# Kernel tuning notes

Hardware: AMD Instinct MI355X
Metric: run time of the kernel (lower is better)

The kernel has to match this reference:

```python
import jax, jax.numpy as jnp
import numpy as np
from jax import lax

STRIDE, PAD, K = 1, 1, 3  # module defaults


def setup_inputs() -> dict:
    key = jax.random.key(0)
    k1, k2, k3, k4 = jax.random.split(key, 4)
    N, C, H, W, O = 8, 64, 112, 112, 64
    n = K * K
    x = jax.random.normal(k1, (N, C, H, W), jnp.float32)
    # kaiming-uniform-ish scale for main conv weight
    weight = jax.random.normal(k2, (O, C, K, K), jnp.float32) * (1.0 / np.sqrt(C * K * K))
    bias = jnp.zeros((O,), jnp.float32)
    # small random offset predictor (original zero-inits; small values exercise bilinear path)
    offset_w = jax.random.normal(k3, (3 * n, C, K, K), jnp.float32) * 0.01
    offset_b = jax.random.normal(k4, (3 * n,), jnp.float32) * 0.01
    return {"x": x, "weight": weight, "bias": bias, "offset_w": offset_w, "offset_b": offset_b}


def _bilinear(x, py, px):
    """Zero-padded bilinear sampling. x:[N,C,H,W]; py,px:[N,n,Ho,Wo] -> [N,C,n,Ho,Wo]."""
    N, C, H, W = x.shape
    xf = x.reshape(N, C, H * W)
    y0 = jnp.floor(py)
    x0 = jnp.floor(px)
    out = jnp.zeros((N, C) + py.shape[1:], x.dtype)
    for dy in (0.0, 1.0):
        for dx in (0.0, 1.0):
            yi = y0 + dy
            xi = x0 + dx
            w = (1.0 - jnp.abs(py - yi)) * (1.0 - jnp.abs(px - xi))
            valid = (yi >= 0) & (yi <= H - 1) & (xi >= 0) & (xi <= W - 1)
            yc = jnp.clip(yi, 0, H - 1).astype(jnp.int32)
            xc = jnp.clip(xi, 0, W - 1).astype(jnp.int32)
            idx = (yc * W + xc).reshape(N, 1, -1)
            g = jnp.take_along_axis(xf, jnp.broadcast_to(idx, (N, C, idx.shape[-1])), axis=2)
            g = g.reshape((N, C) + py.shape[1:])
            out = out + g * jnp.where(valid, w, 0.0)[:, None]
    return out


def reference(x, weight, bias, offset_w, offset_b):
    N, C, H, W = x.shape
    O = weight.shape[0]
    n = K * K
    # offset/mask predictor: 3x3 conv -> [N, 3*n, Ho, Wo]
    raw = lax.conv_general_dilated(
        x, offset_w, (STRIDE, STRIDE), [(PAD, PAD), (PAD, PAD)],
        dimension_numbers=("NCHW", "OIHW", "NCHW"),
    ) + offset_b[None, :, None, None]
    Ho, Wo = raw.shape[2], raw.shape[3]
    off = raw[:, : 2 * n].reshape(N, n, 2, Ho, Wo)       # (dy, dx) per tap
    mask = jax.nn.sigmoid(raw[:, 2 * n :])               # [N, n, Ho, Wo]
    # base sampling grid: p0 + kernel tap position
    tap_y = (jnp.arange(n) // K).astype(jnp.float32)[:, None, None]   # [n,1,1]
    tap_x = (jnp.arange(n) % K).astype(jnp.float32)[:, None, None]
    base_y = (jnp.arange(Ho) * STRIDE - PAD).astype(jnp.float32)[None, :, None] + tap_y  # [n,Ho,1]
    base_x = (jnp.arange(Wo) * STRIDE - PAD).astype(jnp.float32)[None, None, :] + tap_x  # [n,1,Wo]
    py = off[:, :, 0] + base_y[None]   # [N,n,Ho,Wo]
    px = off[:, :, 1] + base_x[None]
    sampled = _bilinear(x, py, px)                       # [N,C,n,Ho,Wo]
    val = sampled * mask[:, None]                        # modulation
    out = jnp.einsum("ncthw,oct->nohw", val, weight.reshape(O, C, n))
    return out + bias[None, :, None, None]
```

## Files before the change

### kernel.cpp

```cpp
#include <hip/hip_runtime.h>
#include <hip/hip_fp16.h>
#include <math.h>

#define NB  8
#define CIN 64
#define HH  112
#define WW  112
#define OC  64
#define HWSZ (HH*WW)
#define NPOS (NB*HWSZ)

#define PR 9
#define PC 22
#define NPOSP (PR*PC)
#define PATCH_CHUNKS (NPOSP*8)

typedef unsigned short u16;
typedef __attribute__((ext_vector_type(8))) _Float16 h8;
typedef __attribute__((ext_vector_type(4))) float floatx4;

#define XT_ELEMS   (NB*HWSZ*CIN)
#define WSWZ_ELEMS (18*4*64*8)
#define OSWZ_ELEMS (18*4*32*8)

union CV { uint4 u; h8 h; };

__device__ __forceinline__ u16 f2h(float f) { return __half_as_ushort(__float2half(f)); }
__device__ __forceinline__ __half2 H2(unsigned v) { union { unsigned u; __half2 h; } c; c.u = v; return c.h; }
__device__ __forceinline__ unsigned U2(__half2 h) { union { unsigned u; __half2 h; } c; c.h = h; return c.u; }
__device__ __forceinline__ unsigned pkh(float lo, float hi) {
    union { __half2 h; unsigned u; } c;
    c.h = __floats2half2_rn(lo, hi);
    return c.u;
}

struct TapW { __half2 w00, w01, w10, w11; };

__global__ __launch_bounds__(256) void transpose_k(
    const float* __restrict__ x, u16* __restrict__ xt)
{
    __shared__ float t[64][65];
    const int n   = blockIdx.y;
    const int hw0 = blockIdx.x * 64;
    const int tid = threadIdx.x;
    const int wv  = tid & 63;
    const int g   = tid >> 6;
    #pragma unroll
    for (int i = 0; i < 16; ++i) {
        const int c = i*4 + g;
        t[c][wv] = x[((size_t)n*CIN + c)*HWSZ + hw0 + wv];
    }
    __syncthreads();
    #pragma unroll
    for (int i = 0; i < 4; ++i) {
        const int unit = i*256 + tid;
        const int cg = unit & 15;
        const int hw = unit >> 4;
        uint2 o;
        o.x = pkh(t[cg*4+0][hw], t[cg*4+1][hw]);
        o.y = pkh(t[cg*4+2][hw], t[cg*4+3][hw]);
        *(uint2*)(xt + ((size_t)n*HWSZ + hw0 + hw)*CIN + cg*4) = o;
    }
}

__global__ __launch_bounds__(256) void wswz_k(
    const float* __restrict__ wgt, const float* __restrict__ offw,
    u16* __restrict__ wswz, u16* __restrict__ oswz)
{
    const int gid = blockIdx.x * 256 + threadIdx.x;
    if (gid < WSWZ_ELEMS) {
        const int j = gid & 7, o = (gid >> 3) & 63, q = (gid >> 9) & 3, s = gid >> 11;
        const int k = s*32 + q*8 + j;
        const int c = k & 63, t = k >> 6;
        wswz[gid] = f2h(wgt[o*576 + c*9 + t]);
    } else {
        const int g2 = gid - WSWZ_ELEMS;
        const int j = g2 & 7, r = (g2 >> 3) & 31, q = (g2 >> 8) & 3, s = g2 >> 10;
        const int k = s*32 + q*8 + j;
        const int c = k & 63, t = k >> 6;
        oswz[g2] = (r < 27) ? f2h(offw[r*576 + c*9 + t]) : (u16)0;
    }
}

#define IML(DST, S_) { \
    const int t_ = (S_) >> 1; \
    const int ty_ = t_/3, tx_ = t_ - 3*ty_; \
    const int r_ = wid + 1 + ty_; \
    const int c_ = m + 1 + tx_; \
    const int pos_ = r_*PC + c_; \
    const int ck_ = ((S_) & 1)*4 + q; \
    DST = *(const uint4*)(patch + pos_*128 + ((ck_ ^ (pos_ & 7)) << 4)); }

#define OFF_MFMA(SRC, S_) { CV cb_; cb_.u = (SRC); \
    const u16* ap_ = oswz + ((S_)*4 + q)*256 + m*8; \
    acc0 = __builtin_amdgcn_mfma_f32_16x16x32_f16(*(const h8*)(ap_),       cb_.h, acc0, 0, 0, 0); \
    acc1 = __builtin_amdgcn_mfma_f32_16x16x32_f16(*(const h8*)(ap_ + 128), cb_.h, acc1, 0, 0, 0); }

#define HALF_STEP(R00, R01, R10, R11, TW, S_) { \
    CV cb_; \
    cb_.u.x = U2(__hfma2(H2((R00).x),(TW).w00, __hfma2(H2((R01).x),(TW).w01, \
              __hfma2(H2((R10).x),(TW).w10, __hmul2(H2((R11).x),(TW).w11))))); \
    cb_.u.y = U2(__hfma2(H2((R00).y),(TW).w00, __hfma2(H2((R01).y),(TW).w01, \
              __hfma2(H2((R10).y),(TW).w10, __hmul2(H2((R11).y),(TW).w11))))); \
    cb_.u.z = U2(__hfma2(H2((R00).z),(TW).w00, __hfma2(H2((R01).z),(TW).w01, \
              __hfma2(H2((R10).z),(TW).w10, __hmul2(H2((R11).z),(TW).w11))))); \
    cb_.u.w = U2(__hfma2(H2((R00).w),(TW).w00, __hfma2(H2((R01).w),(TW).w01, \
              __hfma2(H2((R10).w),(TW).w10, __hmul2(H2((R11).w),(TW).w11))))); \
    const u16* wp_ = wswz + ((S_)*4 + q)*512 + m*8; \
    acc[0] = __builtin_amdgcn_mfma_f32_16x16x32_f16(*(const h8*)(wp_),       cb_.h, acc[0], 0, 0, 0); \
    acc[1] = __builtin_amdgcn_mfma_f32_16x16x32_f16(*(const h8*)(wp_ + 128), cb_.h, acc[1], 0, 0, 0); \
    acc[2] = __builtin_amdgcn_mfma_f32_16x16x32_f16(*(const h8*)(wp_ + 256), cb_.h, acc[2], 0, 0, 0); \
    acc[3] = __builtin_amdgcn_mfma_f32_16x16x32_f16(*(const h8*)(wp_ + 384), cb_.h, acc[3], 0, 0, 0); }

__global__ __launch_bounds__(256)
void dcn_k(
    const u16*  __restrict__ xt,
    const u16*  __restrict__ wswz,
    const u16*  __restrict__ oswz,
    const float* __restrict__ bias,
    const float* __restrict__ offb,
    float* __restrict__ out)
{
    __shared__ uint4 patch4[PATCH_CHUNKS];
    __shared__ float raws[4][32][16];
    __shared__ uint2 prmW[4][9][16];
    __shared__ unsigned prmO[4][9][16];
    char* patch = (char*)patch4;

    const int tid  = threadIdx.x;
    const int lane = tid & 63;
    const int wid  = tid >> 6;
    const int m    = lane & 15;
    const int q    = lane >> 4;

    const int n   = blockIdx.x & 7;
    const int idx = blockIdx.x >> 3;
    const int rg  = idx / 7;
    const int cc  = idx - rg*7;
    const int hoB = rg * 4;
    const int wo0 = cc * 16;
    const int ho  = hoB + wid;
    const u16* xtn = xt + (size_t)n * HWSZ * CIN;

    #pragma unroll
    for (int i = 0; i < 7; ++i) {
        const int u = i*256 + tid;
        if (u < PATCH_CHUNKS) {
            const int pos = u >> 3, ck = u & 7;
            const int pry = pos / PC;
            const int pcx = pos - pry*PC;
            const int gy = hoB - 2 + pry;
            const int gx = wo0 - 2 + pcx;
            uint4 v = {0u,0u,0u,0u};
            if (((unsigned)gy < HH) && ((unsigned)gx < WW))
                v = *(const uint4*)(xtn + (gy*WW + gx)*CIN + ck*8);
            *(uint4*)(patch + pos*128 + ((ck ^ (pos & 7)) << 4)) = v;
        }
    }
    __syncthreads();

    {
        uint4 b[6];
        floatx4 acc0 = {0.f,0.f,0.f,0.f}, acc1 = {0.f,0.f,0.f,0.f};
        #pragma unroll
        for (int s = 0; s < 6; ++s) IML(b[s], s)
        #pragma unroll
        for (int s = 0; s < 6; ++s) {
            uint4 nv; IML(nv, s + 6)
            OFF_MFMA(b[s], s)
            b[s] = nv;
        }
        #pragma unroll
        for (int s = 0; s < 6; ++s) {
            uint4 nv; IML(nv, s + 12)
            OFF_MFMA(b[s], s + 6)
            b[s] = nv;
        }
        #pragma unroll
        for (int s = 0; s < 6; ++s) OFF_MFMA(b[s], s + 12)

        #pragma unroll
        for (int r = 0; r < 4; ++r) {
            raws[wid][q*4 + r][m]      = acc0[r];
            raws[wid][16 + q*4 + r][m] = acc1[r];
        }
    }
    __syncthreads();

    #pragma unroll
    for (int i = 0; i < 3; ++i) {
        const int e = i*64 + lane;
        if (e < 144) {
            const int t = e >> 4;
            const int p = e & 15;
            const int ty = t / 3, tx = t - 3*ty;
            const float py = raws[wid][2*t][p]     + offb[2*t]     + (float)(ho - 1 + ty);
            const float px = raws[wid][2*t + 1][p] + offb[2*t + 1] + (float)(wo0 + p - 1 + tx);
            const float mk = 1.f / (1.f + expf(-(raws[wid][18 + t][p] + offb[18 + t])));
            const float y0f = floorf(py), x0f = floorf(px);
            const float fy = py - y0f, fx = px - x0f;
            const int y0 = (int)y0f, x0 = (int)x0f;
            const float gy = 1.f - fy, gx = 1.f - fx;
            const bool vy0 = (unsigned)y0       < HH;
            const bool vy1 = (unsigned)(y0 + 1) < HH;
            const bool vx0 = (unsigned)x0       < WW;
            const bool vx1 = (unsigned)(x0 + 1) < WW;
            const float w00 = (vy0 && vx0) ? gy*gx*mk : 0.f;
            const float w01 = (vy0 && vx1) ? gy*fx*mk : 0.f;
            const float w10 = (vy1 && vx0) ? fy*gx*mk : 0.f;
            const float w11 = (vy1 && vx1) ? fy*fx*mk : 0.f;
            const int yc0 = min(max(y0, 0), HH-1),  yc1 = min(max(y0+1, 0), HH-1);
            const int xc0 = min(max(x0, 0), WW-1),  xc1 = min(max(x0+1, 0), WW-1);
            const unsigned o00 = (unsigned)((yc0*WW + xc0)*CIN);
            const unsigned dxb = (unsigned)(xc1 - xc0);
            const unsigned dyb = (unsigned)(yc1 - yc0);
            const int r0  = yc0 - (hoB - 2);
            const int c0l = xc0 - (wo0 - 2);
            const bool inp = (r0 >= 0) && (r0 + (int)dyb <= PR-1)
                          && (c0l >= 0) && (c0l + (int)dxb <= PC-1);
            const int pos00 = r0*PC + c0l;
            prmO[wid][t][p] = o00 | (dxb << 20) | (dyb << 21)
                            | (((unsigned)pos00 & 0xFFu) << 22)
                            | (inp ? (1u << 30) : 0u);
            uint2 Wv;
            Wv.x = (unsigned)__half_as_ushort(__float2half(w00))
                 | ((unsigned)__half_as_ushort(__float2half(w01)) << 16);
            Wv.y = (unsigned)__half_as_ushort(__float2half(w10))
                 | ((unsigned)__half_as_ushort(__float2half(w11)) << 16);
            prmW[wid][t][p] = Wv;
        }
    }
    __syncthreads();

    floatx4 acc[4];
    #pragma unroll
    for (int i = 0; i < 4; ++i) acc[i] = (floatx4){0.f,0.f,0.f,0.f};

    const int ch0 = q*8, ch1 = 32 + q*8;

    #pragma unroll
    for (int t = 0; t < 9; ++t) {
        const unsigned Po = prmO[wid][t][m];
        const uint2  Pw = prmW[wid][t][m];
        TapW tw;
        tw.w00 = __half2half2(__ushort_as_half((u16)(Pw.x & 0xFFFFu)));
        tw.w01 = __half2half2(__ushort_as_half((u16)(Pw.x >> 16)));
        tw.w10 = __half2half2(__ushort_as_half((u16)(Pw.y & 0xFFFFu)));
        tw.w11 = __half2half2(__ushort_as_half((u16)(Pw.y >> 16)));
        uint4 g0,g1,g2,g3,g4,g5,g6,g7;
        if (__all((int)((Po >> 30) & 1u))) {
            const int p00 = (int)((Po >> 22) & 0xFFu);
            const int dxb = (int)((Po >> 20) & 1u);
            const int dyb = (int)((Po >> 21) & 1u);
            const int p01 = p00 + dxb;
            const int p10 = p00 + dyb*PC;
            const int p11 = p10 + dxb;
            const int a00 = p00*128 + ((q ^ (p00 & 7)) << 4);
            const int a01 = p01*128 + ((q ^ (p01 & 7)) << 4);
            const int a10 = p10*128 + ((q ^ (p10 & 7)) << 4);
            const int a11 = p11*128 + ((q ^ (p11 & 7)) << 4);
            g0 = *(const uint4*)(patch + a00);
            g1 = *(const uint4*)(patch + a01);
            g2 = *(const uint4*)(patch + a10);
            g3 = *(const uint4*)(patch + a11);
            g4 = *(const uint4*)(patch + (a00 ^ 64));
            g5 = *(const uint4*)(patch + (a01 ^ 64));
            g6 = *(const uint4*)(patch + (a10 ^ 64));
            g7 = *(const uint4*)(patch + (a11 ^ 64));
        } else {
            const int o00 = (int)(Po & 0xFFFFFu);
            const int dx  = (int)((Po >> 20) & 1u) << 6;
            const int dy  = (int)((Po >> 21) & 1u) * (WW*CIN);
            g0 = *(const uint4*)(xtn + o00 + ch0);
            g1 = *(const uint4*)(xtn + o00 + dx + ch0);
            g2 = *(const uint4*)(xtn + o00 + dy + ch0);
            g3 = *(const uint4*)(xtn + o00 + dx + dy + ch0);
            g4 = *(const uint4*)(xtn + o00 + ch1);
            g5 = *(const uint4*)(xtn + o00 + dx + ch1);
            g6 = *(const uint4*)(xtn + o00 + dy + ch1);
            g7 = *(const uint4*)(xtn + o00 + dx + dy + ch1);
        }
        HALF_STEP(g0, g1, g2, g3, tw, 2*t)
        HALF_STEP(g4, g5, g6, g7, tw, 2*t + 1)
    }

    #pragma unroll
    for (int ob = 0; ob < 4; ++ob) {
        #pragma unroll
        for (int r = 0; r < 4; ++r) {
            const int o = ob*16 + q*4 + r;
            out[(((size_t)n*OC + o)*HH + ho)*WW + wo0 + m] = acc[ob][r] + bias[o];
        }
    }
}

extern "C" void kernel_launch(void* const* d_in, const int* in_sizes, int n_in,
                              void* d_out, int out_size, void* d_ws, size_t ws_size,
                              hipStream_t stream)
{
    const float* x    = (const float*)d_in[0];
    const float* wgt  = (const float*)d_in[1];
    const float* bias = (const float*)d_in[2];
    const float* offw = (const float*)d_in[3];
    const float* offb = (const float*)d_in[4];
    float* out = (float*)d_out;

    u16* xt   = (u16*)d_ws;
    u16* wswz = xt + XT_ELEMS;
    u16* oswz = wswz + WSWZ_ELEMS;

    transpose_k<<<dim3(HWSZ/64, NB), 256, 0, stream>>>(x, xt);
    wswz_k<<<dim3((WSWZ_ELEMS + OSWZ_ELEMS)/256), 256, 0, stream>>>(wgt, offw, wswz, oswz);
    dcn_k<<<dim3(NPOS/64), 256, 0, stream>>>(xt, wswz, oswz, bias, offb, out);
}
```

Baseline: 130.6 us.

## Merge prep kernels, shrink patch halo, alias LDS buffers, add fast in-patch path

Measured after the change: 114.8 us. 12.1% less time.

```diff
diff --git a/kernel.cpp b/kernel.cpp
--- a/kernel.cpp
+++ b/kernel.cpp
@@ -10,10 +10,12 @@
 #define HWSZ (HH*WW)
 #define NPOS (NB*HWSZ)
 
-#define PR 9
-#define PC 22
+#define PR 8
+#define PC 21
 #define NPOSP (PR*PC)
 #define PATCH_CHUNKS (NPOSP*8)
+
+#define TP_BLOCKS (HWSZ/64*NB)
 
 typedef unsigned short u16;
 typedef __attribute__((ext_vector_type(8))) _Float16 h8;
@@ -36,49 +38,49 @@
 
 struct TapW { __half2 w00, w01, w10, w11; };
 
-__global__ __launch_bounds__(256) void transpose_k(
-    const float* __restrict__ x, u16* __restrict__ xt)
+__global__ __launch_bounds__(256) void prep_k(
+    const float* __restrict__ x, const float* __restrict__ wgt,
+    const float* __restrict__ offw,
+    u16* __restrict__ xt, u16* __restrict__ wswz, u16* __restrict__ oswz)
 {
     __shared__ float t[64][65];
-    const int n   = blockIdx.y;
-    const int hw0 = blockIdx.x * 64;
     const int tid = threadIdx.x;
-    const int wv  = tid & 63;
-    const int g   = tid >> 6;
-    #pragma unroll
-    for (int i = 0; i < 16; ++i) {
-        const int c = i*4 + g;
-        t[c][wv] = x[((size_t)n*CIN + c)*HWSZ + hw0 + wv];
-    }
-    __syncthreads();
-    #pragma unroll
-    for (int i = 0; i < 4; ++i) {
-        const int unit = i*256 + tid;
-        const int cg = unit & 15;
-        const int hw = unit >> 4;
-        uint2 o;
-        o.x = pkh(t[cg*4+0][hw], t[cg*4+1][hw]);
-        o.y = pkh(t[cg*4+2][hw], t[cg*4+3][hw]);
-        *(uint2*)(xt + ((size_t)n*HWSZ + hw0 + hw)*CIN + cg*4) = o;
-    }
-}
-
-__global__ __launch_bounds__(256) void wswz_k(
-    const float* __restrict__ wgt, const float* __restrict__ offw,
-    u16* __restrict__ wswz, u16* __restrict__ oswz)
-{
-    const int gid = blockIdx.x * 256 + threadIdx.x;
-    if (gid < WSWZ_ELEMS) {
-        const int j = gid & 7, o = (gid >> 3) & 63, q = (gid >> 9) & 3, s = gid >> 11;
-        const int k = s*32 + q*8 + j;
-        const int c = k & 63, t = k >> 6;
-        wswz[gid] = f2h(wgt[o*576 + c*9 + t]);
+    const int bid = blockIdx.x;
+    if (bid < TP_BLOCKS) {
+        const int n   = bid & 7;
+        const int hw0 = (bid >> 3) * 64;
+        const int wv  = tid & 63;
+        const int g   = tid >> 6;
+        #pragma unroll
+        for (int i = 0; i < 16; ++i) {
+            const int c = i*4 + g;
+            t[c][wv] = x[((size_t)n*CIN + c)*HWSZ + hw0 + wv];
+        }
+        __syncthreads();
+        #pragma unroll
+        for (int i = 0; i < 4; ++i) {
+            const int unit = i*256 + tid;
+            const int cg = unit & 15;
+            const int hw = unit >> 4;
+            uint2 o;
+            o.x = pkh(t[cg*4+0][hw], t[cg*4+1][hw]);
+            o.y = pkh(t[cg*4+2][hw], t[cg*4+3][hw]);
+            *(uint2*)(xt + ((size_t)n*HWSZ + hw0 + hw)*CIN + cg*4) = o;
+        }
     } else {
-        const int g2 = gid - WSWZ_ELEMS;
-        const int j = g2 & 7, r = (g2 >> 3) & 31, q = (g2 >> 8) & 3, s = g2 >> 10;
-        const int k = s*32 + q*8 + j;
-        const int c = k & 63, t = k >> 6;
-        oswz[g2] = (r < 27) ? f2h(offw[r*576 + c*9 + t]) : (u16)0;
+        const int gid = (bid - TP_BLOCKS)*256 + tid;
+        if (gid < WSWZ_ELEMS) {
+            const int j = gid & 7, o = (gid >> 3) & 63, q = (gid >> 9) & 3, s = gid >> 11;
+            const int k = s*32 + q*8 + j;
+            const int c = k & 63, tt = k >> 6;
+            wswz[gid] = f2h(wgt[o*576 + c*9 + tt]);
+        } else {
+            const int g2 = gid - WSWZ_ELEMS;
+            const int j = g2 & 7, r = (g2 >> 3) & 31, q = (g2 >> 8) & 3, s = g2 >> 10;
+            const int k = s*32 + q*8 + j;
+            const int c = k & 63, tt = k >> 6;
+            oswz[g2] = (r < 27) ? f2h(offw[r*576 + c*9 + tt]) : (u16)0;
+        }
     }
 }
 
@@ -112,7 +114,14 @@
     acc[2] = __builtin_amdgcn_mfma_f32_16x16x32_f16(*(const h8*)(wp_ + 256), cb_.h, acc[2], 0, 0, 0); \
     acc[3] = __builtin_amdgcn_mfma_f32_16x16x32_f16(*(const h8*)(wp_ + 384), cb_.h, acc[3], 0, 0, 0); }
 
+#define UNPACK_TW(TW, PW) { \
+    (TW).w00 = __half2half2(__ushort_as_half((u16)((PW).x & 0xFFFFu))); \
+    (TW).w01 = __half2half2(__ushort_as_half((u16)((PW).x >> 16))); \
+    (TW).w10 = __half2half2(__ushort_as_half((u16)((PW).y & 0xFFFFu))); \
+    (TW).w11 = __half2half2(__ushort_as_half((u16)((PW).y >> 16))); }
+
 __global__ __launch_bounds__(256)
+__attribute__((amdgpu_waves_per_eu(5, 8)))
 void dcn_k(
     const u16*  __restrict__ xt,
     const u16*  __restrict__ wswz,
@@ -122,10 +131,10 @@
     float* __restrict__ out)
 {
     __shared__ uint4 patch4[PATCH_CHUNKS];
-    __shared__ float raws[4][32][16];
-    __shared__ uint2 prmW[4][9][16];
-    __shared__ unsigned prmO[4][9][16];
+    __shared__ float rawsm[4][32][16];
     char* patch = (char*)patch4;
+    uint2*    prmW = (uint2*)rawsm;
+    unsigned* prmO = (unsigned*)((char*)rawsm + 4608);
 
     const int tid  = threadIdx.x;
     const int lane = tid & 63;
@@ -143,7 +152,7 @@
     const u16* xtn = xt + (size_t)n * HWSZ * CIN;
 
     #pragma unroll
-    for (int i = 0; i < 7; ++i) {
+    for (int i = 0; i < 6; ++i) {
         const int u = i*256 + tid;
         if (u < PATCH_CHUNKS) {
             const int pos = u >> 3, ck = u & 7;
@@ -181,12 +190,24 @@
 
         #pragma unroll
         for (int r = 0; r < 4; ++r) {
-            raws[wid][q*4 + r][m]      = acc0[r];
-            raws[wid][16 + q*4 + r][m] = acc1[r];
+            rawsm[wid][q*4 + r][m]      = acc0[r];
+            rawsm[wid][16 + q*4 + r][m] = acc1[r];
         }
     }
     __syncthreads();
 
+    float vy[3], vx[3], vmk[3];
+    #pragma unroll
+    for (int i = 0; i < 3; ++i) {
+        const int e = i*64 + lane;
+        if (e < 144) {
+            const int t = e >> 4, p = e & 15;
+            vy[i]  = rawsm[wid][2*t][p];
+            vx[i]  = rawsm[wid][2*t + 1][p];
+            vmk[i] = rawsm[wid][18 + t][p];
+        }
+    }
+    __syncthreads();
     #pragma unroll
     for (int i = 0; i < 3; ++i) {
         const int e = i*64 + lane;
@@ -194,9 +215,9 @@
             const int t = e >> 4;
             const int p = e & 15;
             const int ty = t / 3, tx = t - 3*ty;
-            const float py = raws[wid][2*t][p]     + offb[2*t]     + (float)(ho - 1 + ty);
-            const float px = raws[wid][2*t + 1][p] + offb[2*t + 1] + (float)(wo0 + p - 1 + tx);
-            const float mk = 1.f / (1.f + expf(-(raws[wid][18 + t][p] + offb[18 + t])));
+            const float py = vy[i] + offb[2*t]     + (float)(ho - 1 + ty);
+            const float px = vx[i] + offb[2*t + 1] + (float)(wo0 + p - 1 + tx);
+            const float mk = 1.f / (1.f + expf(-(vmk[i] + offb[18 + t])));
             const float y0f = floorf(py), x0f = floorf(px);
             const float fy = py - y0f, fx = px - x0f;
             const int y0 = (int)y0f, x0 = (int)x0f;
@@ -219,7 +240,7 @@
             const bool inp = (r0 >= 0) && (r0 + (int)dyb <= PR-1)
                           && (c0l >= 0) && (c0l + (int)dxb <= PC-1);
             const int pos00 = r0*PC + c0l;
-            prmO[wid][t][p] = o00 | (dxb << 20) | (dyb << 21)
+            prmO[(wid*9 + t)*16 + p] = o00 | (dxb << 20) | (dyb << 21)
                             | (((unsigned)pos00 & 0xFFu) << 22)
                             | (inp ? (1u << 30) : 0u);
             uint2 Wv;
@@ -227,7 +248,7 @@
                  | ((unsigned)__half_as_ushort(__float2half(w01)) << 16);
             Wv.y = (unsigned)__half_as_ushort(__float2half(w10))
                  | ((unsigned)__half_as_ushort(__float2half(w11)) << 16);
-            prmW[wid][t][p] = Wv;
+            prmW[(wid*9 + t)*16 + p] = Wv;
         }
     }
     __syncthreads();
@@ -236,19 +257,20 @@
     #pragma unroll
     for (int i = 0; i < 4; ++i) acc[i] = (floatx4){0.f,0.f,0.f,0.f};
 
-    const int ch0 = q*8, ch1 = 32 + q*8;
-
-    #pragma unroll
-    for (int t = 0; t < 9; ++t) {
-        const unsigned Po = prmO[wid][t][m];
-        const uint2  Pw = prmW[wid][t][m];
-        TapW tw;
-        tw.w00 = __half2half2(__ushort_as_half((u16)(Pw.x & 0xFFFFu)));
-        tw.w01 = __half2half2(__ushort_as_half((u16)(Pw.x >> 16)));
-        tw.w10 = __half2half2(__ushort_as_half((u16)(Pw.y & 0xFFFFu)));
-        tw.w11 = __half2half2(__ushort_as_half((u16)(Pw.y >> 16)));
-        uint4 g0,g1,g2,g3,g4,g5,g6,g7;
-        if (__all((int)((Po >> 30) & 1u))) {
+    const unsigned* PoB = prmO + wid*9*16 + m;
+    const uint2*    PwB = prmW + wid*9*16 + m;
+
+    unsigned band = 0xFFFFFFFFu;
+    #pragma unroll
+    for (int t = 0; t < 9; ++t) band &= PoB[t*16];
+
+    if (__all((int)((band >> 30) & 1u))) {
+        unsigned Po = PoB[0];
+        uint2    Pw = PwB[0];
+        #pragma unroll
+        for (int t = 0; t < 9; ++t) {
+            const unsigned PoN = (t < 8) ? PoB[(t+1)*16] : 0u;
+            const uint2    PwN = (t < 8) ? PwB[(t+1)*16] : Pw;
             const int p00 = (int)((Po >> 22) & 0xFFu);
             const int dxb = (int)((Po >> 20) & 1u);
             const int dyb = (int)((Po >> 21) & 1u);
@@ -259,29 +281,62 @@
             const int a01 = p01*128 + ((q ^ (p01 & 7)) << 4);
             const int a10 = p10*128 + ((q ^ (p10 & 7)) << 4);
             const int a11 = p11*128 + ((q ^ (p11 & 7)) << 4);
-            g0 = *(const uint4*)(patch + a00);
-            g1 = *(const uint4*)(patch + a01);
-            g2 = *(const uint4*)(patch + a10);
-            g3 = *(const uint4*)(patch + a11);
-            g4 = *(const uint4*)(patch + (a00 ^ 64));
-            g5 = *(const uint4*)(patch + (a01 ^ 64));
-            g6 = *(const uint4*)(patch + (a10 ^ 64));
-            g7 = *(const uint4*)(patch + (a11 ^ 64));
-        } else {
-            const int o00 = (int)(Po & 0xFFFFFu);
-            const int dx  = (int)((Po >> 20) & 1u) << 6;
-            const int dy  = (int)((Po >> 21) & 1u) * (WW*CIN);
-            g0 = *(const uint4*)(xtn + o00 + ch0);
-            g1 = *(const uint4*)(xtn + o00 + dx + ch0);
-            g2 = *(const uint4*)(xtn + o00 + dy + ch0);
-            g3 = *(const uint4*)(xtn + o00 + dx + dy + ch0);
-            g4 = *(const uint4*)(xtn + o00 + ch1);
-            g5 = *(const uint4*)(xtn + o00 + dx + ch1);
-            g6 = *(const uint4*)(xtn + o00 + dy + ch1);
-            g7 = *(const uint4*)(xtn + o00 + dx + dy + ch1);
-        }
-        HALF_STEP(g0, g1, g2, g3, tw, 2*t)
-        HALF_STEP(g4, g5, g6, g7, tw, 2*t + 1)
+            const uint4 g0 = *(const uint4*)(patch + a00);
+            const uint4 g1 = *(const uint4*)(patch + a01);
+            const uint4 g2 = *(const uint4*)(patch + a10);
+            const uint4 g3 = *(const uint4*)(patch + a11);
+            const uint4 g4 = *(const uint4*)(patch + (a00 ^ 64));
+            const uint4 g5 = *(const uint4*)(patch + (a01 ^ 64));
+            const uint4 g6 = *(const uint4*)(patch + (a10 ^ 64));
+            const uint4 g7 = *(const uint4*)(patch + (a11 ^ 64));
+            TapW tw; UNPACK_TW(tw, Pw)
+            HALF_STEP(g0, g1, g2, g3, tw, 2*t)
+            HALF_STEP(g4, g5, g6, g7, tw, 2*t + 1)
+            Po = PoN; Pw = PwN;
+        }
+    } else {
+        const int ch0 = q*8, ch1 = 32 + q*8;
+        #pragma unroll
+        for (int t = 0; t < 9; ++t) {
+            const unsigned Po = PoB[t*16];
+            const uint2    Pw = PwB[t*16];
+            TapW tw; UNPACK_TW(tw, Pw)
+            uint4 g0,g1,g2,g3,g4,g5,g6,g7;
+            if (__all((int)((Po >> 30) & 1u))) {
+                const int p00 = (int)((Po >> 22) & 0xFFu);
+                const int dxb = (int)((Po >> 20) & 1u);
+                const int dyb = (int)((Po >> 21) & 1u);
+                const int p01 = p00 + dxb;
+                const int p10 = p00 + dyb*PC;
+                const int p11 = p10 + dxb;
+                const int a00 = p00*128 + ((q ^ (p00 & 7)) << 4);
+                const int a01 = p01*128 + ((q ^ (p01 & 7)) << 4);
+                const int a10 = p10*128 + ((q ^ (p10 & 7)) << 4);
+                const int a11 = p11*128 + ((q ^ (p11 & 7)) << 4);
+                g0 = *(const uint4*)(patch + a00);
+                g1 = *(const uint4*)(patch + a01);
+                g2 = *(const uint4*)(patch + a10);
+                g3 = *(const uint4*)(patch + a11);
+                g4 = *(const uint4*)(patch + (a00 ^ 64));
+                g5 = *(const uint4*)(patch + (a01 ^ 64));
+                g6 = *(const uint4*)(patch + (a10 ^ 64));
+                g7 = *(const uint4*)(patch + (a11 ^ 64));
+            } else {
+                const int o00 = (int)(Po & 0xFFFFFu);
+                const int dx  = (int)((Po >> 20) & 1u) << 6;
+                const int dy  = (int)((Po >> 21) & 1u) * (WW*CIN);
+                g0 = *(const uint4*)(xtn + o00 + ch0);
+                g1 = *(const uint4*)(xtn + o00 + dx + ch0);
+                g2 = *(const uint4*)(xtn + o00 + dy + ch0);
+                g3 = *(const uint4*)(xtn + o00 + dx + dy + ch0);
+                g4 = *(const uint4*)(xtn + o00 + ch1);
+                g5 = *(const uint4*)(xtn + o00 + dx + ch1);
+                g6 = *(const uint4*)(xtn + o00 + dy + ch1);
+                g7 = *(const uint4*)(xtn + o00 + dx + dy + ch1);
+            }
+            HALF_STEP(g0, g1, g2, g3, tw, 2*t)
+            HALF_STEP(g4, g5, g6, g7, tw, 2*t + 1)
+        }
     }
 
     #pragma unroll
@@ -309,7 +364,7 @@
     u16* wswz = xt + XT_ELEMS;
     u16* oswz = wswz + WSWZ_ELEMS;
 
-    transpose_k<<<dim3(HWSZ/64, NB), 256, 0, stream>>>(x, xt);
-    wswz_k<<<dim3((WSWZ_ELEMS + OSWZ_ELEMS)/256), 256, 0, stream>>>(wgt, offw, wswz, oswz);
+    prep_k<<<dim3(TP_BLOCKS + (WSWZ_ELEMS + OSWZ_ELEMS)/256), 256, 0, stream>>>(
+        x, wgt, offw, xt, wswz, oswz);
     dcn_k<<<dim3(NPOS/64), 256, 0, stream>>>(xt, wswz, oswz, bias, offb, out);
 }
```
